# Kernel optimization log

Measured on AMD Instinct MI355X. Metric: run time of the kernel, lower is better.

## Reference

```python
import jax, jax.numpy as jnp
import numpy as np

N_NODES = 50000
IN_DIM = 128
OUT_DIM = 128
HEADS = 4
HEAD_DIM = OUT_DIM // HEADS
N_EDGES = 800000
LN_EPS = 1e-5
NEG_SLOPE = 0.2


def setup_inputs() -> dict:
    key = jax.random.key(0)
    ks = jax.random.split(key, 8)
    x = jax.random.normal(ks[0], (N_NODES, IN_DIM), dtype=jnp.float32)
    edge_index = jax.random.randint(ks[1], (2, N_EDGES), 0, N_NODES, dtype=jnp.int64)
    s = 1.0 / np.sqrt(IN_DIM)
    W = jax.random.uniform(ks[2], (IN_DIM, HEADS * HEAD_DIM), jnp.float32, -s, s)
    att_src = jax.random.uniform(ks[3], (HEADS, HEAD_DIM), jnp.float32, -s, s)
    att_dst = jax.random.uniform(ks[4], (HEADS, HEAD_DIM), jnp.float32, -s, s)
    bias = jnp.zeros((OUT_DIM,), jnp.float32)
    gamma = jnp.ones((OUT_DIM,), jnp.float32)
    beta = jnp.zeros((OUT_DIM,), jnp.float32)
    return {"x": x, "edge_index": edge_index, "W": W, "att_src": att_src,
            "att_dst": att_dst, "bias": bias, "gamma": gamma, "beta": beta}


def reference(x, edge_index, W, att_src, att_dst, bias, gamma, beta):
    N = x.shape[0]
    H, C = att_src.shape
    # add self-loops (PyG GATConv default)
    loops = jnp.arange(N, dtype=edge_index.dtype)
    src = jnp.concatenate([edge_index[0], loops])  # [E+N]
    dst = jnp.concatenate([edge_index[1], loops])

    h = (x @ W).reshape(N, H, C)                      # [N,H,C]
    a_src = jnp.einsum('nhc,hc->nh', h, att_src)      # [N,H]
    a_dst = jnp.einsum('nhc,hc->nh', h, att_dst)

    e = jax.nn.leaky_relu(a_src[src] + a_dst[dst], NEG_SLOPE)   # [E+N,H]
    emax = jax.ops.segment_max(e, dst, num_segments=N)          # [N,H]
    ex = jnp.exp(e - emax[dst])
    denom = jax.ops.segment_sum(ex, dst, num_segments=N)
    alpha = ex / denom[dst]                                     # [E+N,H]

    msg = h[src] * alpha[:, :, None]                            # [E+N,H,C]
    out = jax.ops.segment_sum(msg, dst, num_segments=N).reshape(N, H * C) + bias

    # LayerNorm
    mu = out.mean(-1, keepdims=True)
    var = ((out - mu) ** 2).mean(-1, keepdims=True)
    hn = (out - mu) / jnp.sqrt(var + LN_EPS) * gamma + beta

    # residual is Identity (in_dim == out_dim); GELU exact; dropout = eval identity
    return jax.nn.gelu(hn + x, approximate=False)
```

## Files before the change

### kernel.cpp

```cpp
#include <hip/hip_runtime.h>
#include <math.h>

#define N_NODES 50000
#define HEADS 4
#define NEG_SLOPE 0.2f
#define LN_EPS 1e-5f
#define SLOTS 80
#define GR 32
#define EPB 2048


__device__ __forceinline__ void load_edge(const int* __restrict__ ei, int e, int E,
                                          int is64, int& s, int& d) {
    if (is64) {
        s = ei[2 * e];
        d = ei[2 * (E + e)];
    } else {
        s = ei[e];
        d = ei[E + e];
    }
}

__device__ __forceinline__ int detect_is64(const int* __restrict__ ei, int t, int* s_flag) {
    if (t < 64) {
        int nz = (ei[2 * t + 1] != 0) ? 1 : 0;
        unsigned long long b = __ballot(nz);
        if (t == 0) *s_flag = (b == 0ULL) ? 1 : 0;
    }
    __syncthreads();
    return *s_flag;
}

__device__ __forceinline__ float s8f(unsigned u, int p) {
    return (float)((int)(u << (24 - 8 * p)) >> 24);
}

__device__ __forceinline__ float edge_w(float v) {
    v = v > 0.f ? v : NEG_SLOPE * v;
    return __expf(v);
}

__device__ __forceinline__ void scatter_one(const int* __restrict__ ei, int e, int E,
                                            int is64, int* __restrict__ cnt,
                                            unsigned short* __restrict__ esrc) {
    if (e >= E) return;
    int s, d;
    load_edge(ei, e, E, is64, s, d);
    int p = atomicAdd(&cnt[d], 1);
    if (p < SLOTS) __builtin_nontemporal_store((unsigned short)s, &esrc[d * SLOTS + p]);
}


__global__ __launch_bounds__(256) void gemm_scatter_kernel(
    const float* __restrict__ x, const float* __restrict__ W,
    const float* __restrict__ att_src, const float* __restrict__ att_dst,
    unsigned* __restrict__ hb, float* __restrict__ hscale,
    float* __restrict__ a_src, float* __restrict__ a_dst,
    const int* __restrict__ ei, int E, int nScatter, int nGemm,
    int* __restrict__ cnt, unsigned short* __restrict__ esrc) {
    __shared__ float sX[GR * 128];
    const int t = threadIdx.x;
    const int b = (int)blockIdx.x;

    const bool isScatter = (b % 5) == 0;
    const int rid = isScatter ? (b / 5) : (4 * (b / 5) + (b % 5) - 1);

    if (isScatter) {
        if (rid >= nScatter) return;
        int is64 = detect_is64(ei, t, (int*)sX);
        const int e0 = rid * EPB + t;
#pragma unroll
        for (int u = 0; u < 8; ++u)
            scatter_one(ei, e0 + u * 256, E, is64, cnt, esrc);
        return;
    }

    if (rid >= nGemm) return;
    const int rowBase = rid * GR;
    const int nRows = min(GR, N_NODES - rowBase);

    const float4* x4 = (const float4*)(x + (size_t)rowBase * 128);
    float4* sX4 = (float4*)sX;
    for (int i = t; i < nRows * 32; i += 256) sX4[i] = x4[i];
    __syncthreads();

    const int tx = t & 31;
    const int ty = t >> 5;
    float acc[4][4];
#pragma unroll
    for (int r = 0; r < 4; ++r) { acc[r][0] = acc[r][1] = acc[r][2] = acc[r][3] = 0.f; }

    const float4* W4 = (const float4*)W;
    for (int k = 0; k < 128; k += 4) {
        float4 w0 = W4[(k + 0) * 32 + tx];
        float4 w1 = W4[(k + 1) * 32 + tx];
        float4 w2 = W4[(k + 2) * 32 + tx];
        float4 w3 = W4[(k + 3) * 32 + tx];
#pragma unroll
        for (int r = 0; r < 4; ++r) {
            const float* xr = &sX[(ty * 4 + r) * 128 + k];
            float a0 = xr[0], a1 = xr[1], a2 = xr[2], a3 = xr[3];
            acc[r][0] += a0 * w0.x + a1 * w1.x + a2 * w2.x + a3 * w3.x;
            acc[r][1] += a0 * w0.y + a1 * w1.y + a2 * w2.y + a3 * w3.y;
            acc[r][2] += a0 * w0.z + a1 * w1.z + a2 * w2.z + a3 * w3.z;
            acc[r][3] += a0 * w0.w + a1 * w1.w + a2 * w2.w + a3 * w3.w;
        }
    }

    const float4 as4 = ((const float4*)att_src)[tx];
    const float4 ad4 = ((const float4*)att_dst)[tx];
    const int hd = tx >> 3;
#pragma unroll
    for (int r = 0; r < 4; ++r) {
        int row = rowBase + ty * 4 + r;
        float4 av = make_float4(acc[r][0], acc[r][1], acc[r][2], acc[r][3]);

        float m = fmaxf(fmaxf(fabsf(av.x), fabsf(av.y)),
                        fmaxf(fabsf(av.z), fabsf(av.w)));
#pragma unroll
        for (int o = 1; o < 32; o <<= 1) m = fmaxf(m, __shfl_xor(m, o, 64));
        m = fmaxf(m, 1e-20f);
        const float sc = m * (1.0f / 127.0f);
        const float inv = 127.0f / m;

        if (row < N_NODES) {
            int q0 = __float2int_rn(av.x * inv);
            int q1 = __float2int_rn(av.y * inv);
            int q2 = __float2int_rn(av.z * inv);
            int q3 = __float2int_rn(av.w * inv);
            unsigned pk = (unsigned)(q0 & 255) | ((unsigned)(q1 & 255) << 8) |
                          ((unsigned)(q2 & 255) << 16) | ((unsigned)q3 << 24);
            hb[(size_t)row * 32 + tx] = pk;
            if (tx == 0) hscale[row] = sc;
        }

        float sp = av.x * as4.x + av.y * as4.y + av.z * as4.z + av.w * as4.w;
        float dp = av.x * ad4.x + av.y * ad4.y + av.z * ad4.z + av.w * ad4.w;
#pragma unroll
        for (int o = 1; o < 8; o <<= 1) {
            sp += __shfl_xor(sp, o, 64);
            dp += __shfl_xor(dp, o, 64);
        }
        if ((tx & 7) == 0 && row < N_NODES) {
            a_src[row * 4 + hd] = sp;
            a_dst[row * 4 + hd] = dp;
        }
    }
}

__global__ __launch_bounds__(256) void gat_fused_kernel(
    const int* __restrict__ cnt, const unsigned short* __restrict__ esrc,
    const float* __restrict__ a_src, const float* __restrict__ a_dst,
    const unsigned* __restrict__ hb, const float* __restrict__ hscale,
    const float* __restrict__ bias, const float* __restrict__ x,
    const float* __restrict__ gamma, const float* __restrict__ beta,
    float* __restrict__ out) {
    const int t = threadIdx.x;
    const int l = t & 63;
    const int wv = t >> 6;
    const int g = l >> 4;
    const int j = l & 15;
    const int n = blockIdx.x * 16 + wv * 4 + g;
    const int hh = j >> 2;

    const uint2* hb2 = (const uint2*)hb;

    const float adst_me = a_dst[(n << 2) + hh];
    float ps = edge_w(a_src[(n << 2) + hh] + adst_me);

    uint2 hvS = hb2[(unsigned)(n * 16 + j)];
    {
        const float uS = ps * hscale[n];
        float acc0 = uS * s8f(hvS.x, 0), acc1 = uS * s8f(hvS.x, 1);
        float acc2 = uS * s8f(hvS.x, 2), acc3 = uS * s8f(hvS.x, 3);
        float acc4 = uS * s8f(hvS.y, 0), acc5 = uS * s8f(hvS.y, 1);
        float acc6 = uS * s8f(hvS.y, 2), acc7 = uS * s8f(hvS.y, 3);

        const int deg = min(cnt[n], SLOTS);
        const unsigned short* row = esrc + n * SLOTS;

        for (int base = 0; base < deg; base += 8) {
            const int rem = deg - base;
            uint4 q = *(const uint4*)(row + base);
            int s0 = (int)(q.x & 0xffffu);
            int s1 = (rem > 1) ? (int)(q.x >> 16) : n;
            int s2 = (rem > 2) ? (int)(q.y & 0xffffu) : n;
            int s3 = (rem > 3) ? (int)(q.y >> 16) : n;
            int s4 = (rem > 4) ? (int)(q.z & 0xffffu) : n;
            int s5 = (rem > 5) ? (int)(q.z >> 16) : n;
            int s6 = (rem > 6) ? (int)(q.w & 0xffffu) : n;
            int s7 = (rem > 7) ? (int)(q.w >> 16) : n;

            float b0 = a_src[(s0 << 2) + hh];
            float b1 = a_src[(s1 << 2) + hh];
            float b2 = a_src[(s2 << 2) + hh];
            float b3 = a_src[(s3 << 2) + hh];
            float b4 = a_src[(s4 << 2) + hh];
            float b5 = a_src[(s5 << 2) + hh];
            float b6 = a_src[(s6 << 2) + hh];
            float b7 = a_src[(s7 << 2) + hh];
            float c0 = hscale[s0], c1 = hscale[s1], c2 = hscale[s2], c3 = hscale[s3];
            float c4 = hscale[s4], c5 = hscale[s5], c6 = hscale[s6], c7 = hscale[s7];
            uint2 h0 = hb2[(unsigned)(s0 * 16 + j)];
            uint2 h1 = hb2[(unsigned)(s1 * 16 + j)];
            uint2 h2 = hb2[(unsigned)(s2 * 16 + j)];
            uint2 h3 = hb2[(unsigned)(s3 * 16 + j)];
            uint2 h4 = hb2[(unsigned)(s4 * 16 + j)];
            uint2 h5 = hb2[(unsigned)(s5 * 16 + j)];
            uint2 h6 = hb2[(unsigned)(s6 * 16 + j)];
            uint2 h7 = hb2[(unsigned)(s7 * 16 + j)];

            float w0 = edge_w(b0 + adst_me);
            float w1 = (rem > 1) ? edge_w(b1 + adst_me) : 0.f;
            float w2 = (rem > 2) ? edge_w(b2 + adst_me) : 0.f;
            float w3 = (rem > 3) ? edge_w(b3 + adst_me) : 0.f;
            float w4 = (rem > 4) ? edge_w(b4 + adst_me) : 0.f;
            float w5 = (rem > 5) ? edge_w(b5 + adst_me) : 0.f;
            float w6 = (rem > 6) ? edge_w(b6 + adst_me) : 0.f;
            float w7 = (rem > 7) ? edge_w(b7 + adst_me) : 0.f;
            ps += (w0 + w1 + w2 + w3) + (w4 + w5 + w6 + w7);

            float u0 = w0 * c0, u1 = w1 * c1, u2 = w2 * c2, u3 = w3 * c3;
            float u4 = w4 * c4, u5 = w5 * c5, u6 = w6 * c6, u7 = w7 * c7;

            acc0 += u0 * s8f(h0.x, 0) + u1 * s8f(h1.x, 0) + u2 * s8f(h2.x, 0) + u3 * s8f(h3.x, 0)
                  + u4 * s8f(h4.x, 0) + u5 * s8f(h5.x, 0) + u6 * s8f(h6.x, 0) + u7 * s8f(h7.x, 0);
            acc1 += u0 * s8f(h0.x, 1) + u1 * s8f(h1.x, 1) + u2 * s8f(h2.x, 1) + u3 * s8f(h3.x, 1)
                  + u4 * s8f(h4.x, 1) + u5 * s8f(h5.x, 1) + u6 * s8f(h6.x, 1) + u7 * s8f(h7.x, 1);
            acc2 += u0 * s8f(h0.x, 2) + u1 * s8f(h1.x, 2) + u2 * s8f(h2.x, 2) + u3 * s8f(h3.x, 2)
                  + u4 * s8f(h4.x, 2) + u5 * s8f(h5.x, 2) + u6 * s8f(h6.x, 2) + u7 * s8f(h7.x, 2);
            acc3 += u0 * s8f(h0.x, 3) + u1 * s8f(h1.x, 3) + u2 * s8f(h2.x, 3) + u3 * s8f(h3.x, 3)
                  + u4 * s8f(h4.x, 3) + u5 * s8f(h5.x, 3) + u6 * s8f(h6.x, 3) + u7 * s8f(h7.x, 3);
            acc4 += u0 * s8f(h0.y, 0) + u1 * s8f(h1.y, 0) + u2 * s8f(h2.y, 0) + u3 * s8f(h3.y, 0)
                  + u4 * s8f(h4.y, 0) + u5 * s8f(h5.y, 0) + u6 * s8f(h6.y, 0) + u7 * s8f(h7.y, 0);
            acc5 += u0 * s8f(h0.y, 1) + u1 * s8f(h1.y, 1) + u2 * s8f(h2.y, 1) + u3 * s8f(h3.y, 1)
                  + u4 * s8f(h4.y, 1) + u5 * s8f(h5.y, 1) + u6 * s8f(h6.y, 1) + u7 * s8f(h7.y, 1);
            acc6 += u0 * s8f(h0.y, 2) + u1 * s8f(h1.y, 2) + u2 * s8f(h2.y, 2) + u3 * s8f(h3.y, 2)
                  + u4 * s8f(h4.y, 2) + u5 * s8f(h5.y, 2) + u6 * s8f(h6.y, 2) + u7 * s8f(h7.y, 2);
            acc7 += u0 * s8f(h0.y, 3) + u1 * s8f(h1.y, 3) + u2 * s8f(h2.y, 3) + u3 * s8f(h3.y, 3)
                  + u4 * s8f(h4.y, 3) + u5 * s8f(h5.y, 3) + u6 * s8f(h6.y, 3) + u7 * s8f(h7.y, 3);
        }

        const float inv = 1.0f / ps;
        const float4* bias4 = (const float4*)bias;
        float4 bA = bias4[j * 2], bB = bias4[j * 2 + 1];
        float v0 = acc0 * inv + bA.x, v1 = acc1 * inv + bA.y;
        float v2 = acc2 * inv + bA.z, v3 = acc3 * inv + bA.w;
        float v4 = acc4 * inv + bB.x, v5 = acc5 * inv + bB.y;
        float v6 = acc6 * inv + bB.z, v7 = acc7 * inv + bB.w;

        float s1 = v0 + v1 + v2 + v3 + v4 + v5 + v6 + v7;
        float s2 = v0 * v0 + v1 * v1 + v2 * v2 + v3 * v3 +
                   v4 * v4 + v5 * v5 + v6 * v6 + v7 * v7;
#pragma unroll
        for (int o = 1; o < 16; o <<= 1) {
            s1 += __shfl_xor(s1, o, 64);
            s2 += __shfl_xor(s2, o, 64);
        }
        float mu = s1 * (1.0f / 128.0f);
        float var = s2 * (1.0f / 128.0f) - mu * mu;
        float rstd = rsqrtf(var + LN_EPS);

        const float4* gamma4 = (const float4*)gamma;
        const float4* beta4 = (const float4*)beta;
        const float4* x4 = (const float4*)x;
        float4 gA = gamma4[j * 2], gB = gamma4[j * 2 + 1];
        float4 eA = beta4[j * 2], eB = beta4[j * 2 + 1];
        float4 xA = x4[(size_t)n * 32 + j * 2], xB = x4[(size_t)n * 32 + j * 2 + 1];

        float r0 = (v0 - mu) * rstd * gA.x + eA.x + xA.x;
        float r1 = (v1 - mu) * rstd * gA.y + eA.y + xA.y;
        float r2 = (v2 - mu) * rstd * gA.z + eA.z + xA.z;
        float r3 = (v3 - mu) * rstd * gA.w + eA.w + xA.w;
        float r4 = (v4 - mu) * rstd * gB.x + eB.x + xB.x;
        float r5 = (v5 - mu) * rstd * gB.y + eB.y + xB.y;
        float r6 = (v6 - mu) * rstd * gB.z + eB.z + xB.z;
        float r7 = (v7 - mu) * rstd * gB.w + eB.w + xB.w;

        const float k = 0.70710678118654752440f;
        float4 oA = make_float4(0.5f * r0 * (1.0f + erff(r0 * k)),
                                0.5f * r1 * (1.0f + erff(r1 * k)),
                                0.5f * r2 * (1.0f + erff(r2 * k)),
                                0.5f * r3 * (1.0f + erff(r3 * k)));
        float4 oB = make_float4(0.5f * r4 * (1.0f + erff(r4 * k)),
                                0.5f * r5 * (1.0f + erff(r5 * k)),
                                0.5f * r6 * (1.0f + erff(r6 * k)),
                                0.5f * r7 * (1.0f + erff(r7 * k)));
        float4* out4 = (float4*)out;
        out4[(size_t)n * 32 + j * 2] = oA;
        out4[(size_t)n * 32 + j * 2 + 1] = oB;
    }
}


extern "C" void kernel_launch(void* const* d_in, const int* in_sizes, int n_in,
                              void* d_out, int out_size, void* d_ws, size_t ws_size,
                              hipStream_t stream) {
    const float* x       = (const float*)d_in[0];
    const int*   ei      = (const int*)d_in[1];
    const float* W       = (const float*)d_in[2];
    const float* att_src = (const float*)d_in[3];
    const float* att_dst = (const float*)d_in[4];
    const float* bias    = (const float*)d_in[5];
    const float* gamma   = (const float*)d_in[6];
    const float* beta    = (const float*)d_in[7];
    float* out = (float*)d_out;
    const int E = in_sizes[1] / 2;

    unsigned* hb         = (unsigned*)d_ws;
    float* hscale        = (float*)(hb + (size_t)N_NODES * 32);
    float* a_src         = hscale + N_NODES;
    float* a_dst         = a_src + N_NODES * 4;
    int*   cnt           = (int*)(a_dst + N_NODES * 4);
    unsigned short* esrc = (unsigned short*)(cnt + N_NODES);

    const int nScatter = (E + EPB - 1) / EPB;
    const int nGemm = (N_NODES + GR - 1) / GR;
    int total = 5 * nScatter;
    const int needGemm = 5 * ((nGemm + 3) / 4);
    if (needGemm > total) total = needGemm;

    hipMemsetAsync(cnt, 0, N_NODES * sizeof(int), stream);
    gemm_scatter_kernel<<<total, 256, 0, stream>>>(
        x, W, att_src, att_dst, hb, hscale, a_src, a_dst, ei, E, nScatter, nGemm,
        cnt, esrc);
    gat_fused_kernel<<<N_NODES / 16, 256, 0, stream>>>(cnt, esrc, a_src, a_dst, hb,
                                                       hscale, bias, x, gamma, beta, out);
}
```

Measured before the change: 175.7 us.

## Replace per-edge global atomic scatter with two-pass bucketed binning

```diff
diff --git a/kernel.cpp b/kernel.cpp
--- a/kernel.cpp
+++ b/kernel.cpp
@@ -7,7 +7,11 @@
 #define LN_EPS 1e-5f
 #define SLOTS 80
 #define GR 32
-#define EPB 2048
+#define EPB 1024
+#define NBUCK 256
+#define BK 196
+#define BCAP 4096
+#define LBIN 16
 
 
 __device__ __forceinline__ void load_edge(const int* __restrict__ ei, int e, int E,
@@ -40,42 +44,61 @@
     return __expf(v);
 }
 
-__device__ __forceinline__ void scatter_one(const int* __restrict__ ei, int e, int E,
-                                            int is64, int* __restrict__ cnt,
-                                            unsigned short* __restrict__ esrc) {
-    if (e >= E) return;
-    int s, d;
-    load_edge(ei, e, E, is64, s, d);
-    int p = atomicAdd(&cnt[d], 1);
-    if (p < SLOTS) __builtin_nontemporal_store((unsigned short)s, &esrc[d * SLOTS + p]);
-}
-
-
-__global__ __launch_bounds__(256) void gemm_scatter_kernel(
+
+__global__ __launch_bounds__(256) void gemm_bin_kernel(
     const float* __restrict__ x, const float* __restrict__ W,
     const float* __restrict__ att_src, const float* __restrict__ att_dst,
     unsigned* __restrict__ hb, float* __restrict__ hscale,
     float* __restrict__ a_src, float* __restrict__ a_dst,
-    const int* __restrict__ ei, int E, int nScatter, int nGemm,
-    int* __restrict__ cnt, unsigned short* __restrict__ esrc) {
-    __shared__ float sX[GR * 128];
+    const int* __restrict__ ei, int E, int nBin, int nGemm,
+    int* __restrict__ gcur, unsigned* __restrict__ gbuf) {
+    __shared__ unsigned smem[NBUCK * LBIN + NBUCK];
+    __shared__ int s_flag;
     const int t = threadIdx.x;
     const int b = (int)blockIdx.x;
 
-    const bool isScatter = (b % 5) == 0;
-    const int rid = isScatter ? (b / 5) : (4 * (b / 5) + (b % 5) - 1);
-
-    if (isScatter) {
-        if (rid >= nScatter) return;
-        int is64 = detect_is64(ei, t, (int*)sX);
+    const bool isBin = (b % 3) == 0;
+    const int rid = isBin ? (b / 3) : (2 * (b / 3) + (b % 3) - 1);
+
+    if (isBin) {
+        if (rid >= nBin) return;
+        int* bcnt = (int*)&smem[NBUCK * LBIN];
+        bcnt[t] = 0;
+        __syncthreads();
+        int is64 = detect_is64(ei, t, &s_flag);
+
         const int e0 = rid * EPB + t;
 #pragma unroll
-        for (int u = 0; u < 8; ++u)
-            scatter_one(ei, e0 + u * 256, E, is64, cnt, esrc);
+        for (int u = 0; u < 4; ++u) {
+            int e = e0 + u * 256;
+            if (e >= E) continue;
+            int s, d;
+            load_edge(ei, e, E, is64, s, d);
+            int bk = d / BK;
+            unsigned entry = ((unsigned)(d - bk * BK) << 16) | (unsigned)s;
+            int p = atomicAdd(&bcnt[bk], 1);
+            if (p < LBIN) {
+                smem[bk * LBIN + p] = entry;
+            } else {
+                int gp = atomicAdd(&gcur[bk * 16], 1);
+                if (gp < BCAP) gbuf[(size_t)bk * BCAP + gp] = entry;
+            }
+        }
+        __syncthreads();
+
+        int c = min(bcnt[t], LBIN);
+        if (c > 0) {
+            int base = atomicAdd(&gcur[t * 16], c);
+            for (int i = 0; i < c; ++i) {
+                int idx = base + i;
+                if (idx < BCAP) gbuf[(size_t)t * BCAP + idx] = smem[t * LBIN + i];
+            }
+        }
         return;
     }
 
     if (rid >= nGemm) return;
+    float* sX = (float*)smem;
     const int rowBase = rid * GR;
     const int nRows = min(GR, N_NODES - rowBase);
 
@@ -146,6 +169,29 @@
             a_dst[row * 4 + hd] = dp;
         }
     }
+}
+
+__global__ __launch_bounds__(256) void build_kernel(
+    const unsigned* __restrict__ gbuf, const int* __restrict__ gcur,
+    unsigned short* __restrict__ esrc, int* __restrict__ cnt) {
+    __shared__ int lcnt[BK];
+    const int b = (int)blockIdx.x;
+    const int t = threadIdx.x;
+    if (t < BK) lcnt[t] = 0;
+    __syncthreads();
+
+    const int nE = min(gcur[b * 16], BCAP);
+    const unsigned* src = gbuf + (size_t)b * BCAP;
+    for (int i = t; i < nE; i += 256) {
+        unsigned e = src[i];
+        int dl = (int)(e >> 16);
+        int s = (int)(e & 0xffffu);
+        int p = atomicAdd(&lcnt[dl], 1);
+        if (p < SLOTS) esrc[(size_t)(b * BK + dl) * SLOTS + p] = (unsigned short)s;
+    }
+    __syncthreads();
+    int node = b * BK + t;
+    if (t < BK && node < N_NODES) cnt[node] = lcnt[t];
 }
 
 __global__ __launch_bounds__(256) void gat_fused_kernel(
@@ -169,127 +215,125 @@
     float ps = edge_w(a_src[(n << 2) + hh] + adst_me);
 
     uint2 hvS = hb2[(unsigned)(n * 16 + j)];
-    {
-        const float uS = ps * hscale[n];
-        float acc0 = uS * s8f(hvS.x, 0), acc1 = uS * s8f(hvS.x, 1);
-        float acc2 = uS * s8f(hvS.x, 2), acc3 = uS * s8f(hvS.x, 3);
-        float acc4 = uS * s8f(hvS.y, 0), acc5 = uS * s8f(hvS.y, 1);
-        float acc6 = uS * s8f(hvS.y, 2), acc7 = uS * s8f(hvS.y, 3);
-
-        const int deg = min(cnt[n], SLOTS);
-        const unsigned short* row = esrc + n * SLOTS;
-
-        for (int base = 0; base < deg; base += 8) {
-            const int rem = deg - base;
-            uint4 q = *(const uint4*)(row + base);
-            int s0 = (int)(q.x & 0xffffu);
-            int s1 = (rem > 1) ? (int)(q.x >> 16) : n;
-            int s2 = (rem > 2) ? (int)(q.y & 0xffffu) : n;
-            int s3 = (rem > 3) ? (int)(q.y >> 16) : n;
-            int s4 = (rem > 4) ? (int)(q.z & 0xffffu) : n;
-            int s5 = (rem > 5) ? (int)(q.z >> 16) : n;
-            int s6 = (rem > 6) ? (int)(q.w & 0xffffu) : n;
-            int s7 = (rem > 7) ? (int)(q.w >> 16) : n;
-
-            float b0 = a_src[(s0 << 2) + hh];
-            float b1 = a_src[(s1 << 2) + hh];
-            float b2 = a_src[(s2 << 2) + hh];
-            float b3 = a_src[(s3 << 2) + hh];
-            float b4 = a_src[(s4 << 2) + hh];
-            float b5 = a_src[(s5 << 2) + hh];
-            float b6 = a_src[(s6 << 2) + hh];
-            float b7 = a_src[(s7 << 2) + hh];
-            float c0 = hscale[s0], c1 = hscale[s1], c2 = hscale[s2], c3 = hscale[s3];
-            float c4 = hscale[s4], c5 = hscale[s5], c6 = hscale[s6], c7 = hscale[s7];
-            uint2 h0 = hb2[(unsigned)(s0 * 16 + j)];
-            uint2 h1 = hb2[(unsigned)(s1 * 16 + j)];
-            uint2 h2 = hb2[(unsigned)(s2 * 16 + j)];
-            uint2 h3 = hb2[(unsigned)(s3 * 16 + j)];
-            uint2 h4 = hb2[(unsigned)(s4 * 16 + j)];
-            uint2 h5 = hb2[(unsigned)(s5 * 16 + j)];
-            uint2 h6 = hb2[(unsigned)(s6 * 16 + j)];
-            uint2 h7 = hb2[(unsigned)(s7 * 16 + j)];
-
-            float w0 = edge_w(b0 + adst_me);
-            float w1 = (rem > 1) ? edge_w(b1 + adst_me) : 0.f;
-            float w2 = (rem > 2) ? edge_w(b2 + adst_me) : 0.f;
-            float w3 = (rem > 3) ? edge_w(b3 + adst_me) : 0.f;
-            float w4 = (rem > 4) ? edge_w(b4 + adst_me) : 0.f;
-            float w5 = (rem > 5) ? edge_w(b5 + adst_me) : 0.f;
-            float w6 = (rem > 6) ? edge_w(b6 + adst_me) : 0.f;
-            float w7 = (rem > 7) ? edge_w(b7 + adst_me) : 0.f;
-            ps += (w0 + w1 + w2 + w3) + (w4 + w5 + w6 + w7);
-
-            float u0 = w0 * c0, u1 = w1 * c1, u2 = w2 * c2, u3 = w3 * c3;
-            float u4 = w4 * c4, u5 = w5 * c5, u6 = w6 * c6, u7 = w7 * c7;
-
-            acc0 += u0 * s8f(h0.x, 0) + u1 * s8f(h1.x, 0) + u2 * s8f(h2.x, 0) + u3 * s8f(h3.x, 0)
-                  + u4 * s8f(h4.x, 0) + u5 * s8f(h5.x, 0) + u6 * s8f(h6.x, 0) + u7 * s8f(h7.x, 0);
-            acc1 += u0 * s8f(h0.x, 1) + u1 * s8f(h1.x, 1) + u2 * s8f(h2.x, 1) + u3 * s8f(h3.x, 1)
-                  + u4 * s8f(h4.x, 1) + u5 * s8f(h5.x, 1) + u6 * s8f(h6.x, 1) + u7 * s8f(h7.x, 1);
-            acc2 += u0 * s8f(h0.x, 2) + u1 * s8f(h1.x, 2) + u2 * s8f(h2.x, 2) + u3 * s8f(h3.x, 2)
-                  + u4 * s8f(h4.x, 2) + u5 * s8f(h5.x, 2) + u6 * s8f(h6.x, 2) + u7 * s8f(h7.x, 2);
-            acc3 += u0 * s8f(h0.x, 3) + u1 * s8f(h1.x, 3) + u2 * s8f(h2.x, 3) + u3 * s8f(h3.x, 3)
-                  + u4 * s8f(h4.x, 3) + u5 * s8f(h5.x, 3) + u6 * s8f(h6.x, 3) + u7 * s8f(h7.x, 3);
-            acc4 += u0 * s8f(h0.y, 0) + u1 * s8f(h1.y, 0) + u2 * s8f(h2.y, 0) + u3 * s8f(h3.y, 0)
-                  + u4 * s8f(h4.y, 0) + u5 * s8f(h5.y, 0) + u6 * s8f(h6.y, 0) + u7 * s8f(h7.y, 0);
-            acc5 += u0 * s8f(h0.y, 1) + u1 * s8f(h1.y, 1) + u2 * s8f(h2.y, 1) + u3 * s8f(h3.y, 1)
-                  + u4 * s8f(h4.y, 1) + u5 * s8f(h5.y, 1) + u6 * s8f(h6.y, 1) + u7 * s8f(h7.y, 1);
-            acc6 += u0 * s8f(h0.y, 2) + u1 * s8f(h1.y, 2) + u2 * s8f(h2.y, 2) + u3 * s8f(h3.y, 2)
-                  + u4 * s8f(h4.y, 2) + u5 * s8f(h5.y, 2) + u6 * s8f(h6.y, 2) + u7 * s8f(h7.y, 2);
-            acc7 += u0 * s8f(h0.y, 3) + u1 * s8f(h1.y, 3) + u2 * s8f(h2.y, 3) + u3 * s8f(h3.y, 3)
-                  + u4 * s8f(h4.y, 3) + u5 * s8f(h5.y, 3) + u6 * s8f(h6.y, 3) + u7 * s8f(h7.y, 3);
-        }
-
-        const float inv = 1.0f / ps;
-        const float4* bias4 = (const float4*)bias;
-        float4 bA = bias4[j * 2], bB = bias4[j * 2 + 1];
-        float v0 = acc0 * inv + bA.x, v1 = acc1 * inv + bA.y;
-        float v2 = acc2 * inv + bA.z, v3 = acc3 * inv + bA.w;
-        float v4 = acc4 * inv + bB.x, v5 = acc5 * inv + bB.y;
-        float v6 = acc6 * inv + bB.z, v7 = acc7 * inv + bB.w;
-
-        float s1 = v0 + v1 + v2 + v3 + v4 + v5 + v6 + v7;
-        float s2 = v0 * v0 + v1 * v1 + v2 * v2 + v3 * v3 +
-                   v4 * v4 + v5 * v5 + v6 * v6 + v7 * v7;
-#pragma unroll
-        for (int o = 1; o < 16; o <<= 1) {
-            s1 += __shfl_xor(s1, o, 64);
-            s2 += __shfl_xor(s2, o, 64);
-        }
-        float mu = s1 * (1.0f / 128.0f);
-        float var = s2 * (1.0f / 128.0f) - mu * mu;
-        float rstd = rsqrtf(var + LN_EPS);
-
-        const float4* gamma4 = (const float4*)gamma;
-        const float4* beta4 = (const float4*)beta;
-        const float4* x4 = (const float4*)x;
-        float4 gA = gamma4[j * 2], gB = gamma4[j * 2 + 1];
-        float4 eA = beta4[j * 2], eB = beta4[j * 2 + 1];
-        float4 xA = x4[(size_t)n * 32 + j * 2], xB = x4[(size_t)n * 32 + j * 2 + 1];
-
-        float r0 = (v0 - mu) * rstd * gA.x + eA.x + xA.x;
-        float r1 = (v1 - mu) * rstd * gA.y + eA.y + xA.y;
-        float r2 = (v2 - mu) * rstd * gA.z + eA.z + xA.z;
-        float r3 = (v3 - mu) * rstd * gA.w + eA.w + xA.w;
-        float r4 = (v4 - mu) * rstd * gB.x + eB.x + xB.x;
-        float r5 = (v5 - mu) * rstd * gB.y + eB.y + xB.y;
-        float r6 = (v6 - mu) * rstd * gB.z + eB.z + xB.z;
-        float r7 = (v7 - mu) * rstd * gB.w + eB.w + xB.w;
-
-        const float k = 0.70710678118654752440f;
-        float4 oA = make_float4(0.5f * r0 * (1.0f + erff(r0 * k)),
-                                0.5f * r1 * (1.0f + erff(r1 * k)),
-                                0.5f * r2 * (1.0f + erff(r2 * k)),
-                                0.5f * r3 * (1.0f + erff(r3 * k)));
-        float4 oB = make_float4(0.5f * r4 * (1.0f + erff(r4 * k)),
-                                0.5f * r5 * (1.0f + erff(r5 * k)),
-                                0.5f * r6 * (1.0f + erff(r6 * k)),
-                                0.5f * r7 * (1.0f + erff(r7 * k)));
-        float4* out4 = (float4*)out;
-        out4[(size_t)n * 32 + j * 2] = oA;
-        out4[(size_t)n * 32 + j * 2 + 1] = oB;
-    }
+    const float uS = ps * hscale[n];
+    float acc0 = uS * s8f(hvS.x, 0), acc1 = uS * s8f(hvS.x, 1);
+    float acc2 = uS * s8f(hvS.x, 2), acc3 = uS * s8f(hvS.x, 3);
+    float acc4 = uS * s8f(hvS.y, 0), acc5 = uS * s8f(hvS.y, 1);
+    float acc6 = uS * s8f(hvS.y, 2), acc7 = uS * s8f(hvS.y, 3);
+
+    const int deg = min(cnt[n], SLOTS);
+    const unsigned short* row = esrc + (size_t)n * SLOTS;
+
+    for (int base = 0; base < deg; base += 8) {
+        const int rem = deg - base;
+        uint4 q = *(const uint4*)(row + base);
+        int s0 = (int)(q.x & 0xffffu);
+        int s1 = (rem > 1) ? (int)(q.x >> 16) : n;
+        int s2 = (rem > 2) ? (int)(q.y & 0xffffu) : n;
+        int s3 = (rem > 3) ? (int)(q.y >> 16) : n;
+        int s4 = (rem > 4) ? (int)(q.z & 0xffffu) : n;
+        int s5 = (rem > 5) ? (int)(q.z >> 16) : n;
+        int s6 = (rem > 6) ? (int)(q.w & 0xffffu) : n;
+        int s7 = (rem > 7) ? (int)(q.w >> 16) : n;
+
+        float b0 = a_src[(s0 << 2) + hh];
+        float b1 = a_src[(s1 << 2) + hh];
+        float b2 = a_src[(s2 << 2) + hh];
+        float b3 = a_src[(s3 << 2) + hh];
+        float b4 = a_src[(s4 << 2) + hh];
+        float b5 = a_src[(s5 << 2) + hh];
+        float b6 = a_src[(s6 << 2) + hh];
+        float b7 = a_src[(s7 << 2) + hh];
+        float c0 = hscale[s0], c1 = hscale[s1], c2 = hscale[s2], c3 = hscale[s3];
+        float c4 = hscale[s4], c5 = hscale[s5], c6 = hscale[s6], c7 = hscale[s7];
+        uint2 h0 = hb2[(unsigned)(s0 * 16 + j)];
+        uint2 h1 = hb2[(unsigned)(s1 * 16 + j)];
+        uint2 h2 = hb2[(unsigned)(s2 * 16 + j)];
+        uint2 h3 = hb2[(unsigned)(s3 * 16 + j)];
+        uint2 h4 = hb2[(unsigned)(s4 * 16 + j)];
+        uint2 h5 = hb2[(unsigned)(s5 * 16 + j)];
+        uint2 h6 = hb2[(unsigned)(s6 * 16 + j)];
+        uint2 h7 = hb2[(unsigned)(s7 * 16 + j)];
+
+        float w0 = edge_w(b0 + adst_me);
+        float w1 = (rem > 1) ? edge_w(b1 + adst_me) : 0.f;
+        float w2 = (rem > 2) ? edge_w(b2 + adst_me) : 0.f;
+        float w3 = (rem > 3) ? edge_w(b3 + adst_me) : 0.f;
+        float w4 = (rem > 4) ? edge_w(b4 + adst_me) : 0.f;
+        float w5 = (rem > 5) ? edge_w(b5 + adst_me) : 0.f;
+        float w6 = (rem > 6) ? edge_w(b6 + adst_me) : 0.f;
+        float w7 = (rem > 7) ? edge_w(b7 + adst_me) : 0.f;
+        ps += (w0 + w1 + w2 + w3) + (w4 + w5 + w6 + w7);
+
+        float u0 = w0 * c0, u1 = w1 * c1, u2 = w2 * c2, u3 = w3 * c3;
+        float u4 = w4 * c4, u5 = w5 * c5, u6 = w6 * c6, u7 = w7 * c7;
+
+        acc0 += u0 * s8f(h0.x, 0) + u1 * s8f(h1.x, 0) + u2 * s8f(h2.x, 0) + u3 * s8f(h3.x, 0)
+              + u4 * s8f(h4.x, 0) + u5 * s8f(h5.x, 0) + u6 * s8f(h6.x, 0) + u7 * s8f(h7.x, 0);
+        acc1 += u0 * s8f(h0.x, 1) + u1 * s8f(h1.x, 1) + u2 * s8f(h2.x, 1) + u3 * s8f(h3.x, 1)
+              + u4 * s8f(h4.x, 1) + u5 * s8f(h5.x, 1) + u6 * s8f(h6.x, 1) + u7 * s8f(h7.x, 1);
+        acc2 += u0 * s8f(h0.x, 2) + u1 * s8f(h1.x, 2) + u2 * s8f(h2.x, 2) + u3 * s8f(h3.x, 2)
+              + u4 * s8f(h4.x, 2) + u5 * s8f(h5.x, 2) + u6 * s8f(h6.x, 2) + u7 * s8f(h7.x, 2);
+        acc3 += u0 * s8f(h0.x, 3) + u1 * s8f(h1.x, 3) + u2 * s8f(h2.x, 3) + u3 * s8f(h3.x, 3)
+              + u4 * s8f(h4.x, 3) + u5 * s8f(h5.x, 3) + u6 * s8f(h6.x, 3) + u7 * s8f(h7.x, 3);
+        acc4 += u0 * s8f(h0.y, 0) + u1 * s8f(h1.y, 0) + u2 * s8f(h2.y, 0) + u3 * s8f(h3.y, 0)
+              + u4 * s8f(h4.y, 0) + u5 * s8f(h5.y, 0) + u6 * s8f(h6.y, 0) + u7 * s8f(h7.y, 0);
+        acc5 += u0 * s8f(h0.y, 1) + u1 * s8f(h1.y, 1) + u2 * s8f(h2.y, 1) + u3 * s8f(h3.y, 1)
+              + u4 * s8f(h4.y, 1) + u5 * s8f(h5.y, 1) + u6 * s8f(h6.y, 1) + u7 * s8f(h7.y, 1);
+        acc6 += u0 * s8f(h0.y, 2) + u1 * s8f(h1.y, 2) + u2 * s8f(h2.y, 2) + u3 * s8f(h3.y, 2)
+              + u4 * s8f(h4.y, 2) + u5 * s8f(h5.y, 2) + u6 * s8f(h6.y, 2) + u7 * s8f(h7.y, 2);
+        acc7 += u0 * s8f(h0.y, 3) + u1 * s8f(h1.y, 3) + u2 * s8f(h2.y, 3) + u3 * s8f(h3.y, 3)
+              + u4 * s8f(h4.y, 3) + u5 * s8f(h5.y, 3) + u6 * s8f(h6.y, 3) + u7 * s8f(h7.y, 3);
+    }
+
+    const float inv = 1.0f / ps;
+    const float4* bias4 = (const float4*)bias;
+    float4 bA = bias4[j * 2], bB = bias4[j * 2 + 1];
+    float v0 = acc0 * inv + bA.x, v1 = acc1 * inv + bA.y;
+    float v2 = acc2 * inv + bA.z, v3 = acc3 * inv + bA.w;
+    float v4 = acc4 * inv + bB.x, v5 = acc5 * inv + bB.y;
+    float v6 = acc6 * inv + bB.z, v7 = acc7 * inv + bB.w;
+
+    float s1 = v0 + v1 + v2 + v3 + v4 + v5 + v6 + v7;
+    float s2 = v0 * v0 + v1 * v1 + v2 * v2 + v3 * v3 +
+               v4 * v4 + v5 * v5 + v6 * v6 + v7 * v7;
+#pragma unroll
+    for (int o = 1; o < 16; o <<= 1) {
+        s1 += __shfl_xor(s1, o, 64);
+        s2 += __shfl_xor(s2, o, 64);
+    }
+    float mu = s1 * (1.0f / 128.0f);
+    float var = s2 * (1.0f / 128.0f) - mu * mu;
+    float rstd = rsqrtf(var + LN_EPS);
+
+    const float4* gamma4 = (const float4*)gamma;
+    const float4* beta4 = (const float4*)beta;
+    const float4* x4 = (const float4*)x;
+    float4 gA = gamma4[j * 2], gB = gamma4[j * 2 + 1];
+    float4 eA = beta4[j * 2], eB = beta4[j * 2 + 1];
+    float4 xA = x4[(size_t)n * 32 + j * 2], xB = x4[(size_t)n * 32 + j * 2 + 1];
+
+    float r0 = (v0 - mu) * rstd * gA.x + eA.x + xA.x;
+    float r1 = (v1 - mu) * rstd * gA.y + eA.y + xA.y;
+    float r2 = (v2 - mu) * rstd * gA.z + eA.z + xA.z;
+    float r3 = (v3 - mu) * rstd * gA.w + eA.w + xA.w;
+    float r4 = (v4 - mu) * rstd * gB.x + eB.x + xB.x;
+    float r5 = (v5 - mu) * rstd * gB.y + eB.y + xB.y;
+    float r6 = (v6 - mu) * rstd * gB.z + eB.z + xB.z;
+    float r7 = (v7 - mu) * rstd * gB.w + eB.w + xB.w;
+
+    const float k = 0.70710678118654752440f;
+    float4 oA = make_float4(0.5f * r0 * (1.0f + erff(r0 * k)),
+                            0.5f * r1 * (1.0f + erff(r1 * k)),
+                            0.5f * r2 * (1.0f + erff(r2 * k)),
+                            0.5f * r3 * (1.0f + erff(r3 * k)));
+    float4 oB = make_float4(0.5f * r4 * (1.0f + erff(r4 * k)),
+                            0.5f * r5 * (1.0f + erff(r5 * k)),
+                            0.5f * r6 * (1.0f + erff(r6 * k)),
+                            0.5f * r7 * (1.0f + erff(r7 * k)));
+    float4* out4 = (float4*)out;
+    out4[(size_t)n * 32 + j * 2] = oA;
+    out4[(size_t)n * 32 + j * 2 + 1] = oB;
 }
 
 
@@ -313,17 +357,20 @@
     float* a_dst         = a_src + N_NODES * 4;
     int*   cnt           = (int*)(a_dst + N_NODES * 4);
     unsigned short* esrc = (unsigned short*)(cnt + N_NODES);
-
-    const int nScatter = (E + EPB - 1) / EPB;
+    int*   gcur          = (int*)(esrc + (size_t)N_NODES * SLOTS);
+    unsigned* gbuf       = (unsigned*)(gcur + NBUCK * 16);
+
+    const int nBin  = (E + EPB - 1) / EPB;
     const int nGemm = (N_NODES + GR - 1) / GR;
-    int total = 5 * nScatter;
-    const int needGemm = 5 * ((nGemm + 3) / 4);
+    int total = 3 * nBin;
+    const int needGemm = 3 * ((nGemm + 1) / 2);
     if (needGemm > total) total = needGemm;
 
-    hipMemsetAsync(cnt, 0, N_NODES * sizeof(int), stream);
-    gemm_scatter_kernel<<<total, 256, 0, stream>>>(
-        x, W, att_src, att_dst, hb, hscale, a_src, a_dst, ei, E, nScatter, nGemm,
-        cnt, esrc);
+    hipMemsetAsync(gcur, 0, NBUCK * 16 * sizeof(int), stream);
+    gemm_bin_kernel<<<total, 256, 0, stream>>>(
+        x, W, att_src, att_dst, hb, hscale, a_src, a_dst, ei, E, nBin, nGemm,
+        gcur, gbuf);
+    build_kernel<<<NBUCK, 256, 0, stream>>>(gbuf, gcur, esrc, cnt);
     gat_fused_kernel<<<N_NODES / 16, 256, 0, stream>>>(cnt, esrc, a_src, a_dst, hb,
                                                        hscale, bias, x, gamma, beta, out);
 }
```

New measurement: 177.3 us. About the same (+0.9%).
